# Optimization experiments

Hardware: AMD Instinct MI355X
Metric: run time of the kernel (lower is better)

The kernel has to match this reference:

```python
import jax, jax.numpy as jnp
import numpy as np
from jax import lax

jax.config.update("jax_enable_x64", True)  # hash needs wrapping int64 arithmetic like torch

BATCH, NUM_WINDOWS, FLAT = 32, 1020, 128   # FLAT = num_vars * window_size * k = 4*16*2
VOCAB_ROWS = 2048                           # num_vars * partitions * window_size = 4*32*16
EMBED_DIM = 512
PARTITIONS = 32
BIG_PRIME = 17461204521323


def setup_inputs() -> dict:
    key = jax.random.key(0)
    k1, k2 = jax.random.split(key)
    # Precomputed Fuzzyfier output (mode='indexes', k=2): integer fuzzy-set indexes
    # per window, flattened to [batch, num_windows, num_vars*window_size*k].
    fuzz = jax.random.randint(k1, (BATCH, NUM_WINDOWS, FLAT), 0, PARTITIONS, dtype=jnp.int64)
    embedding = jax.random.normal(k2, (VOCAB_ROWS, EMBED_DIM), dtype=jnp.float32)
    return {"fuzz": fuzz, "embedding": embedding}


def _poly_hash(fuzz):
    # hash_tensor: h = 0; for t in flat: h = (h + t + 1) * P   (int64, wrapping)
    P = jnp.int64(BIG_PRIME)
    xs = jnp.moveaxis(fuzz, -1, 0)  # [FLAT, B, W]
    h0 = jnp.zeros(fuzz.shape[:-1], dtype=jnp.int64)  # [B, W]
    def step(h, t):
        return (h + t + 1) * P, None
    h, _ = lax.scan(step, h0, xs)
    return h  # [B, W] int64


def reference(fuzz, embedding):
    h = _poly_hash(fuzz)
    # Dynamic python-dict vocab replaced by a deterministic GPU-friendly
    # hash->row mapping (mod table size, nonnegative). One gather per token.
    tok = jnp.mod(h, embedding.shape[0])          # [B, W] in [0, VOCAB_ROWS)
    tokens = embedding[tok]                        # [B, W, D]
    return tokens
```

## Files before the change

kernel.cpp:

```cpp
#include <hip/hip_runtime.h>
#include <stdint.h>

constexpr int BATCH       = 32;
constexpr int NUM_WINDOWS = 1020;
constexpr int FLAT        = 128;
constexpr int VOCAB_ROWS  = 2048;
constexpr int EMBED_DIM   = 512;
constexpr unsigned long long BIG_PRIME = 17461204521323ull;

using ull = unsigned long long;
typedef int   vint4   __attribute__((ext_vector_type(4)));
typedef float vfloat4 __attribute__((ext_vector_type(4)));

struct Pows { ull v[FLAT + 1]; };
constexpr Pows make_pows() {
    Pows p{};
    p.v[0] = 1ull;
    for (int i = 1; i <= FLAT; ++i) p.v[i] = p.v[i - 1] * BIG_PRIME;
    return p;
}
__constant__ Pows c_pows = make_pows();

__global__ __launch_bounds__(256) void tokenizer_kernel(
    const int* __restrict__ fuzz,
    const float* __restrict__ emb,
    float* __restrict__ out,
    int n_pairs)
{
    const int gtid = blockIdx.x * blockDim.x + threadIdx.x;
    const int pair = gtid >> 6;
    const int lane = threadIdx.x & 63;
    if (pair >= n_pairs) return;

    const int half = lane >> 5;
    const int j    = lane & 31;
    const int tok_idx = 2 * pair + half;

    const vint4 t = __builtin_nontemporal_load(
        reinterpret_cast<const vint4*>(fuzz + (size_t)pair * (2 * FLAT)) + lane);

    const int e = 4 * j;
    ull h = (ull)(unsigned)(t.x + 1) * c_pows.v[FLAT - e]
          + (ull)(unsigned)(t.y + 1) * c_pows.v[FLAT - e - 1]
          + (ull)(unsigned)(t.z + 1) * c_pows.v[FLAT - e - 2]
          + (ull)(unsigned)(t.w + 1) * c_pows.v[FLAT - e - 3];

    #pragma unroll
    for (int off = 16; off > 0; off >>= 1)
        h += (ull)__shfl_xor((long long)h, off, 64);

    const unsigned tok = (unsigned)(h & (ull)(VOCAB_ROWS - 1));

    const vfloat4* src = reinterpret_cast<const vfloat4*>(emb + (size_t)tok * EMBED_DIM);
    vfloat4*       dst = reinterpret_cast<vfloat4*>(out + (size_t)tok_idx * EMBED_DIM);
    #pragma unroll
    for (int k = 0; k < 4; ++k)
        __builtin_nontemporal_store(src[j + 32 * k], dst + j + 32 * k);
}

extern "C" void kernel_launch(void* const* d_in, const int* in_sizes, int n_in,
                              void* d_out, int out_size, void* d_ws, size_t ws_size,
                              hipStream_t stream) {
    const int*   fuzz = (const int*)d_in[0];
    const float* emb  = (const float*)d_in[1];
    float*       out  = (float*)d_out;

    const int n_tokens = BATCH * NUM_WINDOWS;
    const int n_pairs  = n_tokens / 2;
    const int threads  = 256;
    const int blocks   = (n_pairs * 64 + threads - 1) / threads;

    tokenizer_kernel<<<blocks, threads, 0, stream>>>(fuzz, emb, out, n_pairs);
}
```

Baseline: 94.41 us.

## Split fused hash+gather kernel into separate hash and gather kernels

Breaks the single fused kernel into a hash kernel that writes token ids to workspace and a gather kernel that copies embedding rows with one wavefront per row. Nontemporal loads and stores are replaced with regular ones. The aim is to separate the shuffle-reduction latency from the bandwidth-bound copy. In exchange it adds a second launch and a round trip of token ids through global memory.

```diff
diff --git a/kernel.cpp b/kernel.cpp
--- a/kernel.cpp
+++ b/kernel.cpp
@@ -21,10 +21,9 @@
 }
 __constant__ Pows c_pows = make_pows();
 
-__global__ __launch_bounds__(256) void tokenizer_kernel(
+__global__ __launch_bounds__(256) void hash_kernel(
     const int* __restrict__ fuzz,
-    const float* __restrict__ emb,
-    float* __restrict__ out,
+    int* __restrict__ tok_ids,
     int n_pairs)
 {
     const int gtid = blockIdx.x * blockDim.x + threadIdx.x;
@@ -34,10 +33,8 @@
 
     const int half = lane >> 5;
     const int j    = lane & 31;
-    const int tok_idx = 2 * pair + half;
 
-    const vint4 t = __builtin_nontemporal_load(
-        reinterpret_cast<const vint4*>(fuzz + (size_t)pair * (2 * FLAT)) + lane);
+    const vint4 t = *(reinterpret_cast<const vint4*>(fuzz + (size_t)pair * (2 * FLAT)) + lane);
 
     const int e = 4 * j;
     ull h = (ull)(unsigned)(t.x + 1) * c_pows.v[FLAT - e]
@@ -49,13 +46,27 @@
     for (int off = 16; off > 0; off >>= 1)
         h += (ull)__shfl_xor((long long)h, off, 64);
 
-    const unsigned tok = (unsigned)(h & (ull)(VOCAB_ROWS - 1));
+    if (j == 0)
+        tok_ids[2 * pair + half] = (int)(h & (ull)(VOCAB_ROWS - 1));
+}
+
+__global__ __launch_bounds__(256) void gather_kernel(
+    const int* __restrict__ tok_ids,
+    const float* __restrict__ emb,
+    float* __restrict__ out,
+    int n_tokens)
+{
+    const int gtid = blockIdx.x * blockDim.x + threadIdx.x;
+    const int row  = gtid >> 6;
+    const int lane = threadIdx.x & 63;
+    if (row >= n_tokens) return;
+
+    const int tok = tok_ids[row];
 
     const vfloat4* src = reinterpret_cast<const vfloat4*>(emb + (size_t)tok * EMBED_DIM);
-    vfloat4*       dst = reinterpret_cast<vfloat4*>(out + (size_t)tok_idx * EMBED_DIM);
-    #pragma unroll
-    for (int k = 0; k < 4; ++k)
-        __builtin_nontemporal_store(src[j + 32 * k], dst + j + 32 * k);
+    vfloat4*       dst = reinterpret_cast<vfloat4*>(out + (size_t)row * EMBED_DIM);
+    dst[lane]      = src[lane];
+    dst[lane + 64] = src[lane + 64];
 }
 
 extern "C" void kernel_launch(void* const* d_in, const int* in_sizes, int n_in,
@@ -64,11 +75,15 @@
     const int*   fuzz = (const int*)d_in[0];
     const float* emb  = (const float*)d_in[1];
     float*       out  = (float*)d_out;
+    int*         tok  = (int*)d_ws;
 
     const int n_tokens = BATCH * NUM_WINDOWS;
     const int n_pairs  = n_tokens / 2;
-    const int threads  = 256;
-    const int blocks   = (n_pairs * 64 + threads - 1) / threads;
 
-    tokenizer_kernel<<<blocks, threads, 0, stream>>>(fuzz, emb, out, n_pairs);
+    const int threads = 256;
+    const int hash_blocks   = (n_pairs  * 64 + threads - 1) / threads;
+    const int gather_blocks = (n_tokens * 64 + threads - 1) / threads;
+
+    hash_kernel<<<hash_blocks, threads, 0, stream>>>(fuzz, tok, n_pairs);
+    gather_kernel<<<gather_blocks, threads, 0, stream>>>(tok, emb, out, n_tokens);
 }
```

Result: no change. 95.29 us (+0.9%).
